# Performance work log

Hardware: AMD Instinct MI355X
Metric: run time of the kernel (lower is better)

The kernel has to match this reference:

```python
import jax, jax.numpy as jnp
from jax import lax
import numpy as np

B, N, C = 16, 8192, 256


def farthest_point_sample(pts, npoint):
    # pts: [B, N, 3]. Standard PointNet++ FPS; is_center=True -> start from the
    # point farthest from the centroid (argmax of dist-to-mean).
    b, n, _ = pts.shape
    centroid = pts.mean(axis=1, keepdims=True)                  # [B,1,3]
    d0 = jnp.sum((pts - centroid) ** 2, axis=-1)                # [B,N]
    farthest = jnp.argmax(d0, axis=-1)                          # [B]
    dist = jnp.full((b, n), 1e10, dtype=pts.dtype)

    def step(carry, _):
        dist, far = carry
        cur = jnp.take_along_axis(pts, far[:, None, None], axis=1)  # [B,1,3]
        d = jnp.sum((pts - cur) ** 2, axis=-1)                      # [B,N]
        dist = jnp.minimum(dist, d)
        new_far = jnp.argmax(dist, axis=-1)
        return (dist, new_far), far

    (_, _), idxs = lax.scan(step, (dist, farthest), None, length=npoint)
    return idxs.T  # [B, npoint]


def index_points(x, idx):
    # x: [B, N, D], idx: [B, M] -> [B, M, D]
    return jnp.take_along_axis(x, idx[:, :, None], axis=1)


def setup_inputs() -> dict:
    key = jax.random.key(0)
    k1, k2 = jax.random.split(key)
    points = jax.random.normal(k1, (B, 3, N), dtype=jnp.float32)
    features = jax.random.normal(k2, (B, C, N), dtype=jnp.float32)
    return {"points": points, "features": features, "num_points": 2048}


def reference(points, features, num_points):
    pts = jnp.swapaxes(points, -1, -2)     # [B,N,3]
    feats = jnp.swapaxes(features, -1, -2) # [B,N,C]
    idx = farthest_point_sample(pts, num_points)  # [B,M] int
    sampled_points = index_points(pts, idx)       # [B,M,3]
    sampled_features = index_points(feats, idx)   # [B,M,C]
    return sampled_points, sampled_features
```

## Files before the change

kernel.cpp:

```cpp
#include <hip/hip_runtime.h>
#include <cfloat>

#define BB 16
#define NN 8192
#define CC 256
#define NT 512
#define PPT 16
#define NPAIR (PPT / 2)
#define NWAVES (NT / 64)
#define TBLOCKS 240
#define NTILES (BB * (CC / 64) * (NN / 64))

typedef float    v2f __attribute__((ext_vector_type(2)));
typedef unsigned v2u __attribute__((ext_vector_type(2)));
typedef unsigned uu;
typedef unsigned long long ull;

#define LDS_BARRIER() __asm__ __volatile__("s_waitcnt lgkmcnt(0)\n\ts_barrier" ::: "memory")

struct SmemFPS {
  float px[NN], py[NN], pz[NN];
  ull   key[2][NWAVES];
  float red[NWAVES][3];
  float ctr[3];
};
struct SmemT {
  float tile[64][65];
};
union Smem { SmemFPS f; SmemT t; };

__device__ __forceinline__ v2f pk_sub(v2f a, v2f b) {
  v2f d;
  asm("v_pk_add_f32 %0, %1, %2 neg_lo:[0,1] neg_hi:[0,1]"
      : "=v"(d) : "v"(a), "v"(b));
  return d;
}
__device__ __forceinline__ v2f pk_mul(v2f a, v2f b) {
  v2f d;
  asm("v_pk_mul_f32 %0, %1, %2" : "=v"(d) : "v"(a), "v"(b));
  return d;
}
__device__ __forceinline__ v2f pk_add(v2f a, v2f b) {
  v2f d;
  asm("v_pk_add_f32 %0, %1, %2" : "=v"(d) : "v"(a), "v"(b));
  return d;
}

__device__ __forceinline__ uu umin2(uu a, uu b) { return a < b ? a : b; }
__device__ __forceinline__ uu umax2(uu a, uu b) { return a > b ? a : b; }

__device__ __forceinline__ ull max64(ull a, ull b) { return a > b ? a : b; }

template <int CTRL>
__device__ __forceinline__ ull dpp_max64(ull x) {
  int lo = (int)(uu)x;
  int hi = (int)(uu)(x >> 32);
  int plo = __builtin_amdgcn_update_dpp(0, lo, CTRL, 0xF, 0xF, true);
  int phi = __builtin_amdgcn_update_dpp(0, hi, CTRL, 0xF, 0xF, true);
  ull p = ((ull)(uu)phi << 32) | (uu)plo;
  return max64(x, p);
}

__device__ __forceinline__ ull wave_max63(ull k) {
  k = dpp_max64<0xB1>(k);
  k = dpp_max64<0x4E>(k);
  k = dpp_max64<0x124>(k);
  k = dpp_max64<0x128>(k);
  k = dpp_max64<0x142>(k);
  k = dpp_max64<0x143>(k);
  return k;
}

__global__ __launch_bounds__(NT)
void fps_fused_kernel(const float* __restrict__ pts,
                      const float* __restrict__ feats,
                      float* __restrict__ out_pts,
                      int* __restrict__ idx_out,
                      float* __restrict__ trans, int M, int do_trans) {
  __shared__ Smem sm;
  const int t = threadIdx.x;

  if (blockIdx.x >= BB) {
    if (!do_trans) return;
    for (int tileId = blockIdx.x - BB; tileId < NTILES; tileId += TBLOCKS) {
      int b  = tileId / ((CC / 64) * (NN / 64));
      int r  = tileId % ((CC / 64) * (NN / 64));
      int ct = r / (NN / 64);
      int nt = r % (NN / 64);
      const float* src = feats + ((size_t)b * CC + ct * 64) * NN + nt * 64;
      float* dst = trans + ((size_t)b * NN + nt * 64) * CC + ct * 64;
#pragma unroll
      for (int i = 0; i < 2; ++i) {
        int f = t + i * NT;
        int c = f >> 4, n4 = f & 15;
        float4 v = *(const float4*)(src + (size_t)c * NN + n4 * 4);
        sm.t.tile[c][n4 * 4 + 0] = v.x;
        sm.t.tile[c][n4 * 4 + 1] = v.y;
        sm.t.tile[c][n4 * 4 + 2] = v.z;
        sm.t.tile[c][n4 * 4 + 3] = v.w;
      }
      __syncthreads();
#pragma unroll
      for (int i = 0; i < 2; ++i) {
        int f = t + i * NT;
        int n = f >> 4, c4 = f & 15;
        float4 o;
        o.x = sm.t.tile[c4 * 4 + 0][n];
        o.y = sm.t.tile[c4 * 4 + 1][n];
        o.z = sm.t.tile[c4 * 4 + 2][n];
        o.w = sm.t.tile[c4 * 4 + 3][n];
        *(float4*)(dst + (size_t)n * CC + c4 * 4) = o;
      }
      __syncthreads();
    }
    return;
  }

  const int b = blockIdx.x;
  const int wave = t >> 6;
  const int lane = t & 63;
  const float* base = pts + (size_t)b * 3 * NN;

  v2f px2[NPAIR], py2[NPAIR], pz2[NPAIR];
  v2u dist2[NPAIR];
  const uu INIT = __float_as_uint(1e10f);
#pragma unroll
  for (int j = 0; j < NPAIR; ++j) {
    int n0 = t + (2 * j) * NT;
    int n1 = t + (2 * j + 1) * NT;
    float x0 = base[n0], y0 = base[NN + n0], z0 = base[2 * NN + n0];
    float x1 = base[n1], y1 = base[NN + n1], z1 = base[2 * NN + n1];
    px2[j] = (v2f){x0, x1};
    py2[j] = (v2f){y0, y1};
    pz2[j] = (v2f){z0, z1};
    sm.f.px[n0] = x0; sm.f.py[n0] = y0; sm.f.pz[n0] = z0;
    sm.f.px[n1] = x1; sm.f.py[n1] = y1; sm.f.pz[n1] = z1;
    dist2[j] = (v2u){INIT, INIT};
  }

  float sx = 0.f, sy = 0.f, sz = 0.f;
#pragma unroll
  for (int j = 0; j < NPAIR; ++j) {
    sx += px2[j].x; sx += px2[j].y;
    sy += py2[j].x; sy += py2[j].y;
    sz += pz2[j].x; sz += pz2[j].y;
  }
#pragma unroll
  for (int off = 32; off > 0; off >>= 1) {
    sx += __shfl_xor(sx, off);
    sy += __shfl_xor(sy, off);
    sz += __shfl_xor(sz, off);
  }
  if (lane == 0) { sm.f.red[wave][0] = sx; sm.f.red[wave][1] = sy; sm.f.red[wave][2] = sz; }
  __syncthreads();
  if (t == 0) {
    float gx = 0.f, gy = 0.f, gz = 0.f;
    for (int w = 0; w < NWAVES; ++w) { gx += sm.f.red[w][0]; gy += sm.f.red[w][1]; gz += sm.f.red[w][2]; }
    sm.f.ctr[0] = gx / NN; sm.f.ctr[1] = gy / NN; sm.f.ctr[2] = gz / NN;
  }
  __syncthreads();
  const float ctx = sm.f.ctr[0], cty = sm.f.ctr[1], ctz = sm.f.ctr[2];

  int ep = 0;
  int ci;

  auto reduce_tail = [&](uu v, int bk) {
    ull key = ((ull)v << 32) | (uu)(~(t + (bk << 9)));
    key = wave_max63(key);
    ep ^= 1;
    if (lane == 63) sm.f.key[ep][wave] = key;
    LDS_BARRIER();
    ull kk = sm.f.key[ep][lane & 7];
    kk = dpp_max64<0xB1>(kk);
    kk = dpp_max64<0x4E>(kk);
    kk = dpp_max64<0x124>(kk);
    ci = (int)~(uu)kk;
  };

  {
    v2f c2x = {ctx, ctx}, c2y = {cty, cty}, c2z = {ctz, ctz};
    v2u nd2[NPAIR];
    uu v = 0u;
#pragma unroll
    for (int j = 0; j < NPAIR; ++j) {
      v2f dx = pk_sub(px2[j], c2x);
      v2f dy = pk_sub(py2[j], c2y);
      v2f dz = pk_sub(pz2[j], c2z);
      v2f d = pk_add(pk_add(pk_mul(dx, dx), pk_mul(dy, dy)), pk_mul(dz, dz));
      v2u du = (v2u){__float_as_uint(d.x), __float_as_uint(d.y)};
      nd2[j] = du;
      v = umax2(v, umax2(du.x, du.y));
    }
    int bk = 0;
#pragma unroll
    for (int k = PPT - 1; k >= 0; --k) {
      uu ndk = (k & 1) ? nd2[k >> 1].y : nd2[k >> 1].x;
      if (ndk == v) bk = k;
    }
    reduce_tail(v, bk);
  }

  for (int m = 0; m < M; ++m) {
    float cx = sm.f.px[ci], cy = sm.f.py[ci], cz = sm.f.pz[ci];
    if (t == 0) {
      idx_out[b * M + m] = ci;
      size_t o = ((size_t)b * M + m) * 3;
      out_pts[o] = cx; out_pts[o + 1] = cy; out_pts[o + 2] = cz;
    }
    if (m == M - 1) break;

    v2f c2x = {cx, cx}, c2y = {cy, cy}, c2z = {cz, cz};
    v2u nd2[NPAIR];
    uu v = 0u;
#pragma unroll
    for (int j = 0; j < NPAIR; ++j) {
      v2f dx = pk_sub(px2[j], c2x);
      v2f dy = pk_sub(py2[j], c2y);
      v2f dz = pk_sub(pz2[j], c2z);
      v2f d = pk_add(pk_add(pk_mul(dx, dx), pk_mul(dy, dy)), pk_mul(dz, dz));
      v2u nd;
      nd.x = umin2(dist2[j].x, __float_as_uint(d.x));
      nd.y = umin2(dist2[j].y, __float_as_uint(d.y));
      dist2[j] = nd;
      nd2[j] = nd;
      v = umax2(v, umax2(nd.x, nd.y));
    }
    int bk = 0;
#pragma unroll
    for (int k = PPT - 1; k >= 0; --k) {
      uu ndk = (k & 1) ? nd2[k >> 1].y : nd2[k >> 1].x;
      if (ndk == v) bk = k;
    }
    reduce_tail(v, bk);
  }
}

__global__ __launch_bounds__(256)
void gather_t_kernel(const float* __restrict__ trans,
                     const int* __restrict__ idx,
                     float* __restrict__ out_f, int M) {
  int gm = blockIdx.x * 4 + (threadIdx.x >> 6);
  if (gm >= BB * M) return;
  int lane = threadIdx.x & 63;
  int b = gm / M;
  int n = idx[gm];
  float4 v = *(const float4*)(trans + ((size_t)b * NN + n) * CC + lane * 4);
  *(float4*)(out_f + (size_t)gm * CC + lane * 4) = v;
}

__global__ __launch_bounds__(CC)
void gather_kernel(const float* __restrict__ feats, const int* __restrict__ idx,
                   float* __restrict__ out_f, int M) {
  const int bm = blockIdx.x;
  const int b = bm / M;
  const int n = idx[bm];
  const int c = threadIdx.x;
  out_f[(size_t)bm * CC + c] = feats[((size_t)b * CC + c) * NN + n];
}

extern "C" void kernel_launch(void* const* d_in, const int* in_sizes, int n_in,
                              void* d_out, int out_size, void* d_ws, size_t ws_size,
                              hipStream_t stream) {
  const float* points = (const float*)d_in[0];
  const float* feats  = (const float*)d_in[1];
  int M = out_size / (BB * (3 + CC));
  if (M <= 0) M = 1;

  float* out_pts = (float*)d_out;
  float* out_f   = (float*)d_out + (size_t)BB * M * 3;

  int* idx_ws = (int*)d_ws;
  size_t idx_bytes = (((size_t)BB * M * sizeof(int)) + 255) & ~(size_t)255;
  size_t trans_bytes = (size_t)BB * NN * CC * sizeof(float);
  bool use_t = (ws_size >= idx_bytes + trans_bytes);
  float* trans = (float*)((char*)d_ws + idx_bytes);

  int grid = use_t ? (BB + TBLOCKS) : BB;
  fps_fused_kernel<<<dim3(grid), dim3(NT), 0, stream>>>(
      points, feats, out_pts, idx_ws, trans, M, use_t ? 1 : 0);

  if (use_t) {
    gather_t_kernel<<<dim3((BB * M + 3) / 4), dim3(256), 0, stream>>>(
        trans, idx_ws, out_f, M);
  } else {
    gather_kernel<<<dim3(BB * M), dim3(CC), 0, stream>>>(feats, idx_ws, out_f, M);
  }
}
```

Before: 1.909 ms.

## Morton-sort points into spatial cells and skip distance updates via bounding-box bound

Each FPS block now bins its points into a 512-cell Morton grid, counting-sorts them in LDS so each thread owns 16 spatially coherent points, and records a per-thread bounding box. In each iteration a thread computes a lower bound from the new center to its box and skips the distance update when that bound cannot lower its current max. The aim is to cut the per-iteration ALU work. The cost is a sort prologue, extra registers for original indices, and divergence within waves, since skipping only saves time when a whole wave skips. Tie-breaking now picks the largest complemented index per thread, which keeps smallest-index semantics, but the 0.999999 bound margin adds a slight risk of mismatch.

After: 2.080 ms. +9.0%, slower.

```diff
diff --git a/kernel.cpp b/kernel.cpp
--- a/kernel.cpp
+++ b/kernel.cpp
@@ -10,6 +10,7 @@
 #define NWAVES (NT / 64)
 #define TBLOCKS 240
 #define NTILES (BB * (CC / 64) * (NN / 64))
+#define NCELL 512
 
 typedef float    v2f __attribute__((ext_vector_type(2)));
 typedef unsigned v2u __attribute__((ext_vector_type(2)));
@@ -18,16 +19,19 @@
 
 #define LDS_BARRIER() __asm__ __volatile__("s_waitcnt lgkmcnt(0)\n\ts_barrier" ::: "memory")
 
-struct SmemFPS {
-  float px[NN], py[NN], pz[NN];
+struct SmemSort {
+  float sx[NN], sy[NN], sz[NN];
+  uu    sidx[NN];
+  uu    hist[NCELL], cur[NCELL];
+};
+struct SmemFPS { float px[NN], py[NN], pz[NN]; };
+struct SmemT { float tile[64][65]; };
+union SmemBig { SmemSort s; SmemFPS f; SmemT t; };
+struct SmemCtl {
   ull   key[2][NWAVES];
-  float red[NWAVES][3];
-  float ctr[3];
+  float red[NWAVES][9];
+  float ctr[9];
 };
-struct SmemT {
-  float tile[64][65];
-};
-union Smem { SmemFPS f; SmemT t; };
 
 __device__ __forceinline__ v2f pk_sub(v2f a, v2f b) {
   v2f d;
@@ -71,13 +75,19 @@
   return k;
 }
 
+__device__ __forceinline__ uu sp3(int b) {
+  uu u = (uu)b;
+  return (u & 1u) | ((u & 2u) << 2) | ((u & 4u) << 4);
+}
+
 __global__ __launch_bounds__(NT)
 void fps_fused_kernel(const float* __restrict__ pts,
                       const float* __restrict__ feats,
                       float* __restrict__ out_pts,
                       int* __restrict__ idx_out,
                       float* __restrict__ trans, int M, int do_trans) {
-  __shared__ Smem sm;
+  __shared__ SmemBig smb;
+  __shared__ SmemCtl smc;
   const int t = threadIdx.x;
 
   if (blockIdx.x >= BB) {
@@ -94,10 +104,10 @@
         int f = t + i * NT;
         int c = f >> 4, n4 = f & 15;
         float4 v = *(const float4*)(src + (size_t)c * NN + n4 * 4);
-        sm.t.tile[c][n4 * 4 + 0] = v.x;
-        sm.t.tile[c][n4 * 4 + 1] = v.y;
-        sm.t.tile[c][n4 * 4 + 2] = v.z;
-        sm.t.tile[c][n4 * 4 + 3] = v.w;
+        smb.t.tile[c][n4 * 4 + 0] = v.x;
+        smb.t.tile[c][n4 * 4 + 1] = v.y;
+        smb.t.tile[c][n4 * 4 + 2] = v.z;
+        smb.t.tile[c][n4 * 4 + 3] = v.w;
       }
       __syncthreads();
 #pragma unroll
@@ -105,10 +115,10 @@
         int f = t + i * NT;
         int n = f >> 4, c4 = f & 15;
         float4 o;
-        o.x = sm.t.tile[c4 * 4 + 0][n];
-        o.y = sm.t.tile[c4 * 4 + 1][n];
-        o.z = sm.t.tile[c4 * 4 + 2][n];
-        o.w = sm.t.tile[c4 * 4 + 3][n];
+        o.x = smb.t.tile[c4 * 4 + 0][n];
+        o.y = smb.t.tile[c4 * 4 + 1][n];
+        o.z = smb.t.tile[c4 * 4 + 2][n];
+        o.w = smb.t.tile[c4 * 4 + 3][n];
         *(float4*)(dst + (size_t)n * CC + c4 * 4) = o;
       }
       __syncthreads();
@@ -122,55 +132,161 @@
   const float* base = pts + (size_t)b * 3 * NN;
 
   v2f px2[NPAIR], py2[NPAIR], pz2[NPAIR];
-  v2u dist2[NPAIR];
-  const uu INIT = __float_as_uint(1e10f);
 #pragma unroll
   for (int j = 0; j < NPAIR; ++j) {
     int n0 = t + (2 * j) * NT;
     int n1 = t + (2 * j + 1) * NT;
+    px2[j] = (v2f){base[n0], base[NN + n0] * 0.f + base[n0] * 0.f + base[n0]};
     float x0 = base[n0], y0 = base[NN + n0], z0 = base[2 * NN + n0];
     float x1 = base[n1], y1 = base[NN + n1], z1 = base[2 * NN + n1];
     px2[j] = (v2f){x0, x1};
     py2[j] = (v2f){y0, y1};
     pz2[j] = (v2f){z0, z1};
-    sm.f.px[n0] = x0; sm.f.py[n0] = y0; sm.f.pz[n0] = z0;
-    sm.f.px[n1] = x1; sm.f.py[n1] = y1; sm.f.pz[n1] = z1;
-    dist2[j] = (v2u){INIT, INIT};
   }
 
   float sx = 0.f, sy = 0.f, sz = 0.f;
+  float mnx = FLT_MAX, mny = FLT_MAX, mnz = FLT_MAX;
+  float mxx = -FLT_MAX, mxy = -FLT_MAX, mxz = -FLT_MAX;
 #pragma unroll
   for (int j = 0; j < NPAIR; ++j) {
     sx += px2[j].x; sx += px2[j].y;
     sy += py2[j].x; sy += py2[j].y;
     sz += pz2[j].x; sz += pz2[j].y;
+    mnx = fminf(mnx, fminf(px2[j].x, px2[j].y));
+    mny = fminf(mny, fminf(py2[j].x, py2[j].y));
+    mnz = fminf(mnz, fminf(pz2[j].x, pz2[j].y));
+    mxx = fmaxf(mxx, fmaxf(px2[j].x, px2[j].y));
+    mxy = fmaxf(mxy, fmaxf(py2[j].x, py2[j].y));
+    mxz = fmaxf(mxz, fmaxf(pz2[j].x, pz2[j].y));
   }
 #pragma unroll
   for (int off = 32; off > 0; off >>= 1) {
     sx += __shfl_xor(sx, off);
     sy += __shfl_xor(sy, off);
     sz += __shfl_xor(sz, off);
-  }
-  if (lane == 0) { sm.f.red[wave][0] = sx; sm.f.red[wave][1] = sy; sm.f.red[wave][2] = sz; }
+    mnx = fminf(mnx, __shfl_xor(mnx, off));
+    mny = fminf(mny, __shfl_xor(mny, off));
+    mnz = fminf(mnz, __shfl_xor(mnz, off));
+    mxx = fmaxf(mxx, __shfl_xor(mxx, off));
+    mxy = fmaxf(mxy, __shfl_xor(mxy, off));
+    mxz = fmaxf(mxz, __shfl_xor(mxz, off));
+  }
+  if (lane == 0) {
+    smc.red[wave][0] = sx;  smc.red[wave][1] = sy;  smc.red[wave][2] = sz;
+    smc.red[wave][3] = mnx; smc.red[wave][4] = mny; smc.red[wave][5] = mnz;
+    smc.red[wave][6] = mxx; smc.red[wave][7] = mxy; smc.red[wave][8] = mxz;
+  }
+  if (t < NCELL) smb.s.hist[t] = 0u;
   __syncthreads();
   if (t == 0) {
     float gx = 0.f, gy = 0.f, gz = 0.f;
-    for (int w = 0; w < NWAVES; ++w) { gx += sm.f.red[w][0]; gy += sm.f.red[w][1]; gz += sm.f.red[w][2]; }
-    sm.f.ctr[0] = gx / NN; sm.f.ctr[1] = gy / NN; sm.f.ctr[2] = gz / NN;
-  }
-  __syncthreads();
-  const float ctx = sm.f.ctr[0], cty = sm.f.ctr[1], ctz = sm.f.ctr[2];
+    float lx = FLT_MAX, ly = FLT_MAX, lz = FLT_MAX;
+    float hx = -FLT_MAX, hy = -FLT_MAX, hz = -FLT_MAX;
+    for (int w = 0; w < NWAVES; ++w) {
+      gx += smc.red[w][0]; gy += smc.red[w][1]; gz += smc.red[w][2];
+      lx = fminf(lx, smc.red[w][3]); ly = fminf(ly, smc.red[w][4]); lz = fminf(lz, smc.red[w][5]);
+      hx = fmaxf(hx, smc.red[w][6]); hy = fmaxf(hy, smc.red[w][7]); hz = fmaxf(hz, smc.red[w][8]);
+    }
+    smc.ctr[0] = gx / NN; smc.ctr[1] = gy / NN; smc.ctr[2] = gz / NN;
+    smc.ctr[3] = lx; smc.ctr[4] = ly; smc.ctr[5] = lz;
+    smc.ctr[6] = hx; smc.ctr[7] = hy; smc.ctr[8] = hz;
+  }
+  __syncthreads();
+  const float ctx = smc.ctr[0], cty = smc.ctr[1], ctz = smc.ctr[2];
+  const float lox = smc.ctr[3], loy = smc.ctr[4], loz = smc.ctr[5];
+  const float wxs = smc.ctr[6] - lox, wys = smc.ctr[7] - loy, wzs = smc.ctr[8] - loz;
+  const float sclx = wxs > 0.f ? 8.0f / wxs : 0.f;
+  const float scly = wys > 0.f ? 8.0f / wys : 0.f;
+  const float sclz = wzs > 0.f ? 8.0f / wzs : 0.f;
+
+  uu code[PPT];
+#pragma unroll
+  for (int k = 0; k < PPT; ++k) {
+    float x = (k & 1) ? px2[k >> 1].y : px2[k >> 1].x;
+    float y = (k & 1) ? py2[k >> 1].y : py2[k >> 1].x;
+    float z = (k & 1) ? pz2[k >> 1].y : pz2[k >> 1].x;
+    float fx = (x - lox) * sclx; fx = fx > 7.f ? 7.f : (fx < 0.f ? 0.f : fx);
+    float fy = (y - loy) * scly; fy = fy > 7.f ? 7.f : (fy < 0.f ? 0.f : fy);
+    float fz = (z - loz) * sclz; fz = fz > 7.f ? 7.f : (fz < 0.f ? 0.f : fz);
+    code[k] = sp3((int)fx) | (sp3((int)fy) << 1) | (sp3((int)fz) << 2);
+    atomicAdd(&smb.s.hist[code[k]], 1u);
+  }
+  __syncthreads();
+
+  if (wave == 0) {
+    uu h[8]; uu s = 0u;
+#pragma unroll
+    for (int j2 = 0; j2 < 8; ++j2) { h[j2] = smb.s.hist[lane * 8 + j2]; s += h[j2]; }
+    uu inc = s;
+#pragma unroll
+    for (int d = 1; d < 64; d <<= 1) { uu tt = __shfl_up(inc, d); if (lane >= d) inc += tt; }
+    uu run = inc - s;
+#pragma unroll
+    for (int j2 = 0; j2 < 8; ++j2) { smb.s.cur[lane * 8 + j2] = run; run += h[j2]; }
+  }
+  __syncthreads();
+
+#pragma unroll
+  for (int k = 0; k < PPT; ++k) {
+    float x = (k & 1) ? px2[k >> 1].y : px2[k >> 1].x;
+    float y = (k & 1) ? py2[k >> 1].y : py2[k >> 1].x;
+    float z = (k & 1) ? pz2[k >> 1].y : pz2[k >> 1].x;
+    uu p = atomicAdd(&smb.s.cur[code[k]], 1u);
+    smb.s.sx[p] = x; smb.s.sy[p] = y; smb.s.sz[p] = z;
+    smb.s.sidx[p] = ~(uu)(t + k * NT);
+  }
+  __syncthreads();
+
+  v2u dist2[NPAIR];
+  uu nidx[PPT];
+  const uu INIT = __float_as_uint(1e10f);
+  const int base16 = t * PPT;
+#pragma unroll
+  for (int j = 0; j < NPAIR; ++j) {
+    int p0 = base16 + 2 * j, p1 = p0 + 1;
+    px2[j] = (v2f){smb.s.sx[p0], smb.s.sx[p1]};
+    py2[j] = (v2f){smb.s.sy[p0], smb.s.sy[p1]};
+    pz2[j] = (v2f){smb.s.sz[p0], smb.s.sz[p1]};
+    nidx[2 * j] = smb.s.sidx[p0];
+    nidx[2 * j + 1] = smb.s.sidx[p1];
+    dist2[j] = (v2u){INIT, INIT};
+  }
+  float bxlo = FLT_MAX, bylo = FLT_MAX, bzlo = FLT_MAX;
+  float bxhi = -FLT_MAX, byhi = -FLT_MAX, bzhi = -FLT_MAX;
+#pragma unroll
+  for (int j = 0; j < NPAIR; ++j) {
+    bxlo = fminf(bxlo, fminf(px2[j].x, px2[j].y));
+    bylo = fminf(bylo, fminf(py2[j].x, py2[j].y));
+    bzlo = fminf(bzlo, fminf(pz2[j].x, pz2[j].y));
+    bxhi = fmaxf(bxhi, fmaxf(px2[j].x, px2[j].y));
+    byhi = fmaxf(byhi, fmaxf(py2[j].x, py2[j].y));
+    bzhi = fmaxf(bzhi, fmaxf(pz2[j].x, pz2[j].y));
+  }
+  uu myv = INIT, myc = 0u;
+#pragma unroll
+  for (int k = 0; k < PPT; ++k) myc = umax2(myc, nidx[k]);
+  __syncthreads();
+
+#pragma unroll
+  for (int k = 0; k < PPT; ++k) {
+    uu o = ~nidx[k];
+    float x = (k & 1) ? px2[k >> 1].y : px2[k >> 1].x;
+    float y = (k & 1) ? py2[k >> 1].y : py2[k >> 1].x;
+    float z = (k & 1) ? pz2[k >> 1].y : pz2[k >> 1].x;
+    smb.f.px[o] = x; smb.f.py[o] = y; smb.f.pz[o] = z;
+  }
+  __syncthreads();
 
   int ep = 0;
   int ci;
 
-  auto reduce_tail = [&](uu v, int bk) {
-    ull key = ((ull)v << 32) | (uu)(~(t + (bk << 9)));
+  auto reduce_tail = [&](uu v, uu c) {
+    ull key = ((ull)v << 32) | c;
     key = wave_max63(key);
     ep ^= 1;
-    if (lane == 63) sm.f.key[ep][wave] = key;
+    if (lane == 63) smc.key[ep][wave] = key;
     LDS_BARRIER();
-    ull kk = sm.f.key[ep][lane & 7];
+    ull kk = smc.key[ep][lane & 7];
     kk = dpp_max64<0xB1>(kk);
     kk = dpp_max64<0x4E>(kk);
     kk = dpp_max64<0x124>(kk);
@@ -191,17 +307,17 @@
       nd2[j] = du;
       v = umax2(v, umax2(du.x, du.y));
     }
-    int bk = 0;
-#pragma unroll
-    for (int k = PPT - 1; k >= 0; --k) {
-      uu ndk = (k & 1) ? nd2[k >> 1].y : nd2[k >> 1].x;
-      if (ndk == v) bk = k;
-    }
-    reduce_tail(v, bk);
+    uu c = 0u;
+#pragma unroll
+    for (int j = 0; j < NPAIR; ++j) {
+      c = umax2(c, nd2[j].x == v ? nidx[2 * j] : 0u);
+      c = umax2(c, nd2[j].y == v ? nidx[2 * j + 1] : 0u);
+    }
+    reduce_tail(v, c);
   }
 
   for (int m = 0; m < M; ++m) {
-    float cx = sm.f.px[ci], cy = sm.f.py[ci], cz = sm.f.pz[ci];
+    float cx = smb.f.px[ci], cy = smb.f.py[ci], cz = smb.f.pz[ci];
     if (t == 0) {
       idx_out[b * M + m] = ci;
       size_t o = ((size_t)b * M + m) * 3;
@@ -209,29 +325,38 @@
     }
     if (m == M - 1) break;
 
-    v2f c2x = {cx, cx}, c2y = {cy, cy}, c2z = {cz, cz};
-    v2u nd2[NPAIR];
-    uu v = 0u;
-#pragma unroll
-    for (int j = 0; j < NPAIR; ++j) {
-      v2f dx = pk_sub(px2[j], c2x);
-      v2f dy = pk_sub(py2[j], c2y);
-      v2f dz = pk_sub(pz2[j], c2z);
-      v2f d = pk_add(pk_add(pk_mul(dx, dx), pk_mul(dy, dy)), pk_mul(dz, dz));
-      v2u nd;
-      nd.x = umin2(dist2[j].x, __float_as_uint(d.x));
-      nd.y = umin2(dist2[j].y, __float_as_uint(d.y));
-      dist2[j] = nd;
-      nd2[j] = nd;
-      v = umax2(v, umax2(nd.x, nd.y));
-    }
-    int bk = 0;
-#pragma unroll
-    for (int k = PPT - 1; k >= 0; --k) {
-      uu ndk = (k & 1) ? nd2[k >> 1].y : nd2[k >> 1].x;
-      if (ndk == v) bk = k;
-    }
-    reduce_tail(v, bk);
+    float dxx = fmaxf(fmaxf(bxlo - cx, cx - bxhi), 0.f);
+    float dyy = fmaxf(fmaxf(bylo - cy, cy - byhi), 0.f);
+    float dzz = fmaxf(fmaxf(bzlo - cz, cz - bzhi), 0.f);
+    float lb2 = (dxx * dxx + dyy * dyy) + dzz * dzz;
+    bool need = (lb2 * 0.999999f) < __uint_as_float(myv);
+
+    if (need) {
+      v2f c2x = {cx, cx}, c2y = {cy, cy}, c2z = {cz, cz};
+      v2u nd2[NPAIR];
+      uu v = 0u;
+#pragma unroll
+      for (int j = 0; j < NPAIR; ++j) {
+        v2f dx = pk_sub(px2[j], c2x);
+        v2f dy = pk_sub(py2[j], c2y);
+        v2f dz = pk_sub(pz2[j], c2z);
+        v2f d = pk_add(pk_add(pk_mul(dx, dx), pk_mul(dy, dy)), pk_mul(dz, dz));
+        v2u nd;
+        nd.x = umin2(dist2[j].x, __float_as_uint(d.x));
+        nd.y = umin2(dist2[j].y, __float_as_uint(d.y));
+        dist2[j] = nd;
+        nd2[j] = nd;
+        v = umax2(v, umax2(nd.x, nd.y));
+      }
+      uu c = 0u;
+#pragma unroll
+      for (int j = 0; j < NPAIR; ++j) {
+        c = umax2(c, nd2[j].x == v ? nidx[2 * j] : 0u);
+        c = umax2(c, nd2[j].y == v ? nidx[2 * j + 1] : 0u);
+      }
+      myv = v; myc = c;
+    }
+    reduce_tail(myv, myc);
   }
 }
 
```
